# Kernel optimization log

Measured on AMD Instinct MI355X. Metric: run time of the kernel, lower is better.

Reference implementation:

```python
import jax, jax.numpy as jnp
import numpy as np

D_MODEL = 1024
NUM_HEADS = 16
D_K = D_MODEL // NUM_HEADS
THETA = 10000.0
MAX_SEQ_LEN = 2048
BATCH = 2
SEQ = 2048


def setup_inputs() -> dict:
    key = jax.random.key(0)
    ks = jax.random.split(key, 5)
    std = np.sqrt(2.0 / (D_MODEL + D_MODEL)).astype(np.float32)
    x = jax.random.normal(ks[0], (BATCH, SEQ, D_MODEL), dtype=jnp.float32)
    Wq = jax.random.normal(ks[1], (D_MODEL, D_MODEL), dtype=jnp.float32) * std
    Wk = jax.random.normal(ks[2], (D_MODEL, D_MODEL), dtype=jnp.float32) * std
    Wv = jax.random.normal(ks[3], (D_MODEL, D_MODEL), dtype=jnp.float32) * std
    Wo = jax.random.normal(ks[4], (D_MODEL, D_MODEL), dtype=jnp.float32) * std
    token_positions = jnp.arange(SEQ, dtype=jnp.int32)
    return {"x": x, "token_positions": token_positions,
            "Wq": Wq, "Wk": Wk, "Wv": Wv, "Wo": Wo}


def _rope_tables(positions):
    # freqs: [d_k/2]; angles: [seq, d_k/2]
    freqs = 1.0 / (THETA ** (jnp.arange(0, D_K, 2, dtype=jnp.float32) / D_K))
    angles = positions.astype(jnp.float32)[:, None] * freqs[None, :]
    return jnp.cos(angles), jnp.sin(angles)


def _apply_rope(t, cos, sin):
    # t: [b, h, s, d_k]; cos/sin: [s, d_k/2]; interleaved pair rotation
    x1 = t[..., 0::2]
    x2 = t[..., 1::2]
    r1 = x1 * cos - x2 * sin
    r2 = x1 * sin + x2 * cos
    return jnp.stack([r1, r2], axis=-1).reshape(t.shape)


def reference(x, token_positions, Wq, Wk, Wv, Wo):
    b, s, _ = x.shape
    # projections: y = x W^T
    q = jnp.einsum('bsi,oi->bso', x, Wq)
    k = jnp.einsum('bsi,oi->bso', x, Wk)
    v = jnp.einsum('bsi,oi->bso', x, Wv)
    # split heads: [b, h, s, d]
    q = q.reshape(b, s, NUM_HEADS, D_K).transpose(0, 2, 1, 3)
    k = k.reshape(b, s, NUM_HEADS, D_K).transpose(0, 2, 1, 3)
    v = v.reshape(b, s, NUM_HEADS, D_K).transpose(0, 2, 1, 3)
    cos, sin = _rope_tables(token_positions)
    q = _apply_rope(q, cos, sin)
    k = _apply_rope(k, cos, sin)
    scale = jnp.asarray(D_K, jnp.float32) ** 0.5
    scores = jnp.einsum('bhqd,bhkd->bhqk', q, k) / scale
    causal = jnp.tril(jnp.ones((s, s), dtype=bool))
    scores = jnp.where(causal, scores, -jnp.inf)
    attn = jax.nn.softmax(scores.astype(jnp.float32), axis=-1).astype(scores.dtype)
    out = jnp.einsum('bhqk,bhkd->bhqd', attn, v)
    out = out.transpose(0, 2, 1, 3).reshape(b, s, D_MODEL)
    return jnp.einsum('bsi,oi->bso', out, Wo)
```

## Files before the change

### kernel.cpp

```cpp
#include <hip/hip_runtime.h>
#include <stdint.h>

#define D_MODEL 1024
#define NH      16
#define DKH     64
#define SEQLEN  2048
#define BATCH   2
#define KDIM    1024

typedef __attribute__((ext_vector_type(8))) short          short8;
typedef __attribute__((ext_vector_type(4))) short          bf16x4;
typedef __attribute__((ext_vector_type(8))) unsigned short ushort8;
typedef __attribute__((ext_vector_type(4))) unsigned short usht4;
typedef __attribute__((ext_vector_type(4))) float          f32x4;

#define QSCALE 0.18033688011112042f

__device__ __forceinline__ unsigned short f2bf(float f) {
    union { float f; unsigned u; } v; v.f = f;
    unsigned u = v.u;
    unsigned r = (u + 0x7FFFu + ((u >> 16) & 1u)) >> 16;
    return (unsigned short)r;
}
__device__ __forceinline__ unsigned fbits(float f) {
    union { float f; unsigned u; } v; v.f = f; return v.u;
}

__device__ __forceinline__ void gload_lds16(const unsigned short* g, unsigned short* l) {
    __builtin_amdgcn_global_load_lds(
        (__attribute__((address_space(1))) void*)(g),
        (__attribute__((address_space(3))) void*)(l), 16, 0, 0);
}

__global__ void cvt_all(const float* __restrict__ X,  const float* __restrict__ Wq,
                        const float* __restrict__ Wk, const float* __restrict__ Wv,
                        const float* __restrict__ Wo, const int* __restrict__ pos,
                        unsigned short* __restrict__ Xb,  unsigned short* __restrict__ Wqb,
                        unsigned short* __restrict__ Wkb, unsigned short* __restrict__ Wvb,
                        unsigned short* __restrict__ Wob, float2* __restrict__ tbl) {
    const int z = blockIdx.y;
    if (z == 5) {
        int i = blockIdx.x * 256 + threadIdx.x;
        if (i < 65536) {
            int s = i >> 5, j = i & 31;
            float freq = expf(-((float)(2 * j) * (1.0f / 64.0f)) * 9.210340371976184f);
            float ang = (float)pos[s] * freq;
            float sn, cn;
            sincosf(ang, &sn, &cn);
            tbl[i] = make_float2(cn, sn);
        }
        return;
    }
    const float* src; unsigned short* dst; int n;
    if (z == 0)      { src = X;  dst = Xb;  n = 4194304; }
    else if (z == 1) { src = Wq; dst = Wqb; n = 1048576; }
    else if (z == 2) { src = Wk; dst = Wkb; n = 1048576; }
    else if (z == 3) { src = Wv; dst = Wvb; n = 1048576; }
    else             { src = Wo; dst = Wob; n = 1048576; }
    int i = (blockIdx.x * 256 + threadIdx.x) * 8;
    if (i >= n) return;
    float4 a = *(const float4*)(src + i);
    float4 b = *(const float4*)(src + i + 4);
    ushort8 o;
    o[0] = f2bf(a.x); o[1] = f2bf(a.y); o[2] = f2bf(a.z); o[3] = f2bf(a.w);
    o[4] = f2bf(b.x); o[5] = f2bf(b.y); o[6] = f2bf(b.z); o[7] = f2bf(b.w);
    *(ushort8*)(dst + i) = o;
}

__device__ __forceinline__ void gemm_core_128(
    const unsigned short* __restrict__ A, const unsigned short* __restrict__ W,
    unsigned short* a_lds, unsigned short* b_lds,
    int m0, int n0, f32x4 acc[4][4])
{
    const int tid  = threadIdx.x;
    const int lane = tid & 63;
    const int w    = tid >> 6;
    const int quad = lane >> 4;
    const int l16  = lane & 15;
    const int wm   = w & 1, wn = w >> 1;

    const int row_in = lane >> 3;
    const int cg     = ((lane & 7) ^ row_in) * 8;

    #pragma unroll
    for (int mi = 0; mi < 4; mi++)
        #pragma unroll
        for (int ni = 0; ni < 4; ni++) {
            f32x4 z = {0.f, 0.f, 0.f, 0.f};
            acc[mi][ni] = z;
        }

    const int x7 = l16 & 7;

    for (int kk = 0; kk < KDIM; kk += 64) {
        __syncthreads();
        #pragma unroll
        for (int j = 0; j < 4; ++j) {
            int c = w * 4 + j;
            gload_lds16(A + (size_t)(m0 + c * 8 + row_in) * KDIM + kk + cg, &a_lds[c * 512]);
            gload_lds16(W + (size_t)(n0 + c * 8 + row_in) * KDIM + kk + cg, &b_lds[c * 512]);
        }
        __syncthreads();

        short8 af[2][4], bf[2][4];
        #pragma unroll
        for (int kk2 = 0; kk2 < 2; kk2++)
            #pragma unroll
            for (int i = 0; i < 4; i++) {
                int g = (kk2 * 4 + quad) ^ x7;
                af[kk2][i] = *(const short8*)&a_lds[(wm * 64 + i * 16 + l16) * 64 + g * 8];
                bf[kk2][i] = *(const short8*)&b_lds[(wn * 64 + i * 16 + l16) * 64 + g * 8];
            }
        #pragma unroll
        for (int kk2 = 0; kk2 < 2; kk2++)
            #pragma unroll
            for (int mi = 0; mi < 4; mi++)
                #pragma unroll
                for (int ni = 0; ni < 4; ni++)
                    acc[mi][ni] = __builtin_amdgcn_mfma_f32_16x16x32_bf16(af[kk2][mi], bf[kk2][ni], acc[mi][ni], 0, 0, 0);
    }
}

__device__ __forceinline__ void gemm_core_128x64_db(
    const unsigned short* __restrict__ A, const unsigned short* __restrict__ W,
    unsigned short* a_lds, unsigned short* b_lds,
    int m0, int n0, f32x4 acc[4][2])
{
    const int tid  = threadIdx.x;
    const int lane = tid & 63;
    const int w    = tid >> 6;
    const int quad = lane >> 4;
    const int l16  = lane & 15;
    const int wm   = w & 1, wn = w >> 1;

    const int row_in = lane >> 3;
    const int cg     = ((lane & 7) ^ row_in) * 8;

    #pragma unroll
    for (int mi = 0; mi < 4; mi++)
        #pragma unroll
        for (int ni = 0; ni < 2; ni++) {
            f32x4 z = {0.f, 0.f, 0.f, 0.f};
            acc[mi][ni] = z;
        }

    const int x7 = l16 & 7;

    #pragma unroll
    for (int j = 0; j < 4; ++j) {
        int c = w * 4 + j;
        gload_lds16(A + (size_t)(m0 + c * 8 + row_in) * KDIM + cg, &a_lds[c * 512]);
    }
    #pragma unroll
    for (int j = 0; j < 2; ++j) {
        int c = w * 2 + j;
        gload_lds16(W + (size_t)(n0 + c * 8 + row_in) * KDIM + cg, &b_lds[c * 512]);
    }
    __syncthreads();

    int cur = 0;
    for (int kk = 0; kk < KDIM; kk += 64) {
        if (kk + 64 < KDIM) {
            const int nxt = cur ^ 1;
            #pragma unroll
            for (int j = 0; j < 4; ++j) {
                int c = w * 4 + j;
                gload_lds16(A + (size_t)(m0 + c * 8 + row_in) * KDIM + kk + 64 + cg,
                            &a_lds[nxt * 8192 + c * 512]);
            }
            #pragma unroll
            for (int j = 0; j < 2; ++j) {
                int c = w * 2 + j;
                gload_lds16(W + (size_t)(n0 + c * 8 + row_in) * KDIM + kk + 64 + cg,
                            &b_lds[nxt * 4096 + c * 512]);
            }
        }

        const unsigned short* al = &a_lds[cur * 8192];
        const unsigned short* bl = &b_lds[cur * 4096];
        short8 af[2][4], bf[2][2];
        #pragma unroll
        for (int kk2 = 0; kk2 < 2; kk2++) {
            #pragma unroll
            for (int i = 0; i < 4; i++) {
                int g = (kk2 * 4 + quad) ^ x7;
                af[kk2][i] = *(const short8*)&al[(wm * 64 + i * 16 + l16) * 64 + g * 8];
            }
            #pragma unroll
            for (int i = 0; i < 2; i++) {
                int g = (kk2 * 4 + quad) ^ x7;
                bf[kk2][i] = *(const short8*)&bl[(wn * 32 + i * 16 + l16) * 64 + g * 8];
            }
        }
        #pragma unroll
        for (int kk2 = 0; kk2 < 2; kk2++)
            #pragma unroll
            for (int mi = 0; mi < 4; mi++)
                #pragma unroll
                for (int ni = 0; ni < 2; ni++)
                    acc[mi][ni] = __builtin_amdgcn_mfma_f32_16x16x32_bf16(af[kk2][mi], bf[kk2][ni], acc[mi][ni], 0, 0, 0);

        __syncthreads();
        cur ^= 1;
    }
}

__global__ __launch_bounds__(256, 2)
void gemm_qkv(const unsigned short* __restrict__ X,
              const unsigned short* __restrict__ Wq,
              const unsigned short* __restrict__ Wk,
              const unsigned short* __restrict__ Wv,
              const float2* __restrict__ tbl,
              unsigned short* __restrict__ q_ws,
              unsigned short* __restrict__ k_ws,
              unsigned short* __restrict__ v_ws)
{
    __shared__ __align__(16) unsigned short a_lds[128 * 64];
    __shared__ __align__(16) unsigned short b_lds[128 * 64];
    __shared__ __align__(16) unsigned short t_lds[32 * 136];

    const int z = blockIdx.z;
    const unsigned short* W = (z == 0) ? Wq : ((z == 1) ? Wk : Wv);
    const int m0 = blockIdx.x * 128, n0 = blockIdx.y * 128;

    f32x4 acc[4][4];
    gemm_core_128(X, W, a_lds, b_lds, m0, n0, acc);

    const int tid  = threadIdx.x;
    const int lane = tid & 63;
    const int w    = tid >> 6;
    const int quad = lane >> 4;
    const int l16  = lane & 15;
    const int wm   = w & 1, wn = w >> 1;

    if (z == 2) {
        const int bx = m0 >> 11;
        const int c_local_w = wn * 16 + l16;
        const int rd_c = tid >> 3;
        const int rd_s = (tid & 7) * 16;
        #pragma unroll
        for (int ni = 0; ni < 4; ni++) {
            __syncthreads();
            #pragma unroll
            for (int mi = 0; mi < 4; mi++) {
                usht4 v4;
                #pragma unroll
                for (int r = 0; r < 4; r++) v4[r] = f2bf(acc[mi][ni][r]);
                *(usht4*)&t_lds[c_local_w * 136 + wm * 64 + mi * 16 + quad * 4] = v4;
            }
            __syncthreads();
            int col = n0 + (rd_c >> 4) * 64 + ni * 16 + (rd_c & 15);
            int h = col >> 6, d = col & 63;
            size_t base = (size_t)(bx * NH + h) * DKH * SEQLEN + (size_t)d * SEQLEN
                        + (m0 & 2047) + rd_s;
            ushort8 x0 = *(ushort8*)&t_lds[rd_c * 136 + rd_s];
            ushort8 x1 = *(ushort8*)&t_lds[rd_c * 136 + rd_s + 8];
            *(ushort8*)&v_ws[base]     = x0;
            *(ushort8*)&v_ws[base + 8] = x1;
        }
    } else {
        unsigned short* dst = (z == 0) ? q_ws : k_ws;
        const float sc = (z == 0) ? QSCALE : 1.0f;
        #pragma unroll
        for (int mi = 0; mi < 4; mi++)
            #pragma unroll
            for (int ni = 0; ni < 4; ni++)
                #pragma unroll
                for (int r = 0; r < 4; r++) {
                    int row = m0 + wm * 64 + mi * 16 + quad * 4 + r;
                    int col = n0 + wn * 64 + ni * 16 + l16;
                    int b = row >> 11, s = row & 2047;
                    int h = col >> 6,  d = col & 63;
                    float val = acc[mi][ni][r];
                    float other = __shfl_xor(val, 1);
                    float2 cs = tbl[s * 32 + (d >> 1)];
                    float rv = (d & 1) ? (other * cs.y + val * cs.x)
                                       : (val * cs.x - other * cs.y);
                    dst[(size_t)(b * NH + h) * SEQLEN * DKH + (size_t)s * DKH + d] =
                        f2bf(rv * sc);
                }
    }
}

__global__ __launch_bounds__(512, 2)
void attn_kernel(const unsigned short* __restrict__ q_ws,
                 const unsigned short* __restrict__ k_ws,
                 const unsigned short* __restrict__ v_ws,
                 unsigned short* __restrict__ ao)
{
    __shared__ __align__(16) unsigned short smem[17920];
    unsigned short* k_lds = smem;
    unsigned short* v_lds = smem + 128 * 72;
    float* redO = (float*)smem;
    float* redL = redO + 8192;

    const int bh  = blockIdx.x;
    const int y   = blockIdx.y;
    const int qt2 = (y < 8) ? y : (23 - y);
    const int tid = threadIdx.x, lane = tid & 63, w = tid >> 6;
    const int quad = lane >> 4, l16 = lane & 15;
    const int g   = w >> 2;
    const int w4  = w & 3;
    const int nf0 = g * 4;

    const size_t kqbase = (size_t)bh * SEQLEN * DKH;
    const size_t vbase  = (size_t)bh * DKH * SEQLEN;
    const int b = bh >> 4, h = bh & 15;

    const int krow = tid >> 3, kcol = (tid & 7) * 8;
    const int vrow = tid >> 4, vcol = (tid & 15) * 8;

    const int q0  = qt2 * 128;
    const int nt  = qt2 + 1;
    const int qwbase = q0 + w4 * 32;

    short8 aq[2][2];
    #pragma unroll
    for (int st = 0; st < 2; st++)
        #pragma unroll
        for (int kc = 0; kc < 2; kc++)
            aq[st][kc] = *(const short8*)(q_ws + kqbase +
                (size_t)(qwbase + st * 16 + l16) * DKH + kc * 32 + quad * 8);

    f32x4 o_acc[2][4];
    #pragma unroll
    for (int st = 0; st < 2; st++)
        #pragma unroll
        for (int df = 0; df < 4; df++) { f32x4 z = {0.f,0.f,0.f,0.f}; o_acc[st][df] = z; }
    float lsum[2] = {0.f, 0.f};

    ushort8 kreg[2], vreg[2];
    #pragma unroll
    for (int rr = 0; rr < 2; ++rr) {
        kreg[rr] = *(const ushort8*)(k_ws + kqbase + (size_t)(krow + rr * 64) * DKH + kcol);
        vreg[rr] = *(const ushort8*)(v_ws + vbase + (size_t)(vrow + rr * 32) * SEQLEN + vcol);
    }

    for (int t = 0; t < nt; ++t) {
        const int s0 = t * 128;
        __syncthreads();
        #pragma unroll
        for (int rr = 0; rr < 2; ++rr) {
            *(ushort8*)&k_lds[(krow + rr * 64) * 72 + kcol]  = kreg[rr];
            *(ushort8*)&v_lds[(vrow + rr * 32) * 136 + vcol] = vreg[rr];
        }
        __syncthreads();
        if (t < nt - 1) {
            int s1 = s0 + 128;
            #pragma unroll
            for (int rr = 0; rr < 2; ++rr) {
                kreg[rr] = *(const ushort8*)(k_ws + kqbase + (size_t)(s1 + krow + rr * 64) * DKH + kcol);
                vreg[rr] = *(const ushort8*)(v_ws + vbase + (size_t)(vrow + rr * 32) * SEQLEN + s1 + vcol);
            }
        }

        const bool diag = (t == nt - 1);
        #pragma unroll
        for (int nfi = 0; nfi < 4; nfi++) {
            const int nf = nf0 + nfi;
            short8 kf0 = *(const short8*)&k_lds[(nf * 16 + l16) * 72 + 0 * 32 + quad * 8];
            short8 kf1 = *(const short8*)&k_lds[(nf * 16 + l16) * 72 + 1 * 32 + quad * 8];
            bf16x4 vf[4];
            #pragma unroll
            for (int df = 0; df < 4; df++)
                vf[df] = *(const bf16x4*)&v_lds[(df * 16 + l16) * 136 + nf * 16 + quad * 4];

            #pragma unroll
            for (int st = 0; st < 2; st++) {
                f32x4 s = {0.f,0.f,0.f,0.f};
                s = __builtin_amdgcn_mfma_f32_16x16x32_bf16(kf0, aq[st][0], s, 0, 0, 0);
                s = __builtin_amdgcn_mfma_f32_16x16x32_bf16(kf1, aq[st][1], s, 0, 0, 0);

                if (diag) {
                    int qg = qwbase + st * 16 + l16;
                    int kg = s0 + nf * 16 + quad * 4;
                    #pragma unroll
                    for (int r = 0; r < 4; r++)
                        s[r] = (kg + r <= qg) ? __builtin_amdgcn_exp2f(s[r]) : 0.f;
                } else {
                    #pragma unroll
                    for (int r = 0; r < 4; r++)
                        s[r] = __builtin_amdgcn_exp2f(s[r]);
                }
                lsum[st] += s[0] + s[1] + s[2] + s[3];

                union { unsigned u[2]; bf16x4 v; } pk;
                pk.u[0] = __builtin_amdgcn_perm(fbits(s[1]), fbits(s[0]), 0x07060302u);
                pk.u[1] = __builtin_amdgcn_perm(fbits(s[3]), fbits(s[2]), 0x07060302u);

                #pragma unroll
                for (int df = 0; df < 4; df++)
                    o_acc[st][df] = __builtin_amdgcn_mfma_f32_16x16x16bf16_1k(vf[df], pk.v, o_acc[st][df], 0, 0, 0);
            }
        }
    }

    __syncthreads();
    if (g == 1) {
        #pragma unroll
        for (int st = 0; st < 2; st++) {
            #pragma unroll
            for (int df = 0; df < 4; df++)
                *(f32x4*)&redO[(((w4 * 2 + st) * 4 + df) << 8) + lane * 4] = o_acc[st][df];
            redL[(w4 * 2 + st) * 64 + lane] = lsum[st];
        }
    }
    __syncthreads();
    if (g == 0) {
        #pragma unroll
        for (int st = 0; st < 2; st++) {
            #pragma unroll
            for (int df = 0; df < 4; df++) {
                f32x4 o1 = *(const f32x4*)&redO[(((w4 * 2 + st) * 4 + df) << 8) + lane * 4];
                o_acc[st][df] += o1;
            }
            float rs = lsum[st] + redL[(w4 * 2 + st) * 64 + lane];
            rs += __shfl_xor(rs, 16);
            rs += __shfl_xor(rs, 32);
            float inv = 1.0f / rs;
            int qg = qwbase + st * 16 + l16;
            #pragma unroll
            for (int df = 0; df < 4; df++) {
                usht4 ov;
                #pragma unroll
                for (int r = 0; r < 4; r++) ov[r] = f2bf(o_acc[st][df][r] * inv);
                *(usht4*)&ao[(size_t)(b * SEQLEN + qg) * D_MODEL + h * DKH + df * 16 + quad * 4] = ov;
            }
        }
    }
}

__global__ __launch_bounds__(256, 2)
void gemm_out(const unsigned short* __restrict__ AO,
              const unsigned short* __restrict__ Wo,
              float* __restrict__ out)
{
    __shared__ __align__(16) unsigned short a_lds[2 * 128 * 64];
    __shared__ __align__(16) unsigned short b_lds[2 * 64 * 64];

    const int m0 = blockIdx.x * 128, n0 = blockIdx.y * 64;
    f32x4 acc[4][2];
    gemm_core_128x64_db(AO, Wo, a_lds, b_lds, m0, n0, acc);

    const int lane = threadIdx.x & 63;
    const int w    = threadIdx.x >> 6;
    const int quad = lane >> 4;
    const int l16  = lane & 15;
    const int wm   = w & 1, wn = w >> 1;

    #pragma unroll
    for (int mi = 0; mi < 4; mi++)
        #pragma unroll
        for (int ni = 0; ni < 2; ni++)
            #pragma unroll
            for (int r = 0; r < 4; r++) {
                int row = m0 + wm * 64 + mi * 16 + quad * 4 + r;
                int col = n0 + wn * 32 + ni * 16 + l16;
                out[(size_t)row * D_MODEL + col] = acc[mi][ni][r];
            }
}

extern "C" void kernel_launch(void* const* d_in, const int* in_sizes, int n_in,
                              void* d_out, int out_size, void* d_ws, size_t ws_size,
                              hipStream_t stream) {
    const float* X  = (const float*)d_in[0];
    const int*   pos = (const int*)d_in[1];
    const float* Wq = (const float*)d_in[2];
    const float* Wk = (const float*)d_in[3];
    const float* Wv = (const float*)d_in[4];
    const float* Wo = (const float*)d_in[5];
    float* out = (float*)d_out;

    unsigned short* Xb  = (unsigned short*)d_ws;
    unsigned short* Wqb = Xb + 4194304;
    unsigned short* Wkb = Wqb + 1048576;
    unsigned short* Wvb = Wkb + 1048576;
    unsigned short* Wob = Wvb + 1048576;
    unsigned short* q_ws = Wob + 1048576;
    unsigned short* k_ws = q_ws + 4194304;
    unsigned short* v_ws = k_ws + 4194304;
    unsigned short* ao   = v_ws + 4194304;
    float2* tbl = (float2*)(ao + 4194304);

    cvt_all<<<dim3(2048, 6), dim3(256), 0, stream>>>(X, Wq, Wk, Wv, Wo, pos,
                                                     Xb, Wqb, Wkb, Wvb, Wob, tbl);
    gemm_qkv<<<dim3(32, 8, 3), dim3(256), 0, stream>>>(Xb, Wqb, Wkb, Wvb, tbl, q_ws, k_ws, v_ws);
    attn_kernel<<<dim3(32, 16), dim3(512), 0, stream>>>(q_ws, k_ws, v_ws, ao);
    gemm_out<<<dim3(32, 16), dim3(256), 0, stream>>>(ao, Wob, out);
}
```

Baseline: 163.1 us.

## Use 512-thread QKV GEMM blocks and double-buffer K/V tiles in attention

The QKV projection kernel now launches 512 threads (8 waves) per 128x128 tile. Each wave computes a 64x32 sub-tile with fewer accumulators, which aims to raise occupancy and latency hiding; the V-transpose epilogue is reworked to match. The attention kernel double-buffers its K/V LDS tiles, so each step needs one barrier instead of two and the next tile's LDS store overlaps the current compute. The cost is doubled attention LDS use, which may cut blocks per CU, and more barrier participants in the GEMM.

```diff
diff --git a/kernel.cpp b/kernel.cpp
--- a/kernel.cpp
+++ b/kernel.cpp
@@ -67,60 +67,6 @@
     *(ushort8*)(dst + i) = o;
 }
 
-__device__ __forceinline__ void gemm_core_128(
-    const unsigned short* __restrict__ A, const unsigned short* __restrict__ W,
-    unsigned short* a_lds, unsigned short* b_lds,
-    int m0, int n0, f32x4 acc[4][4])
-{
-    const int tid  = threadIdx.x;
-    const int lane = tid & 63;
-    const int w    = tid >> 6;
-    const int quad = lane >> 4;
-    const int l16  = lane & 15;
-    const int wm   = w & 1, wn = w >> 1;
-
-    const int row_in = lane >> 3;
-    const int cg     = ((lane & 7) ^ row_in) * 8;
-
-    #pragma unroll
-    for (int mi = 0; mi < 4; mi++)
-        #pragma unroll
-        for (int ni = 0; ni < 4; ni++) {
-            f32x4 z = {0.f, 0.f, 0.f, 0.f};
-            acc[mi][ni] = z;
-        }
-
-    const int x7 = l16 & 7;
-
-    for (int kk = 0; kk < KDIM; kk += 64) {
-        __syncthreads();
-        #pragma unroll
-        for (int j = 0; j < 4; ++j) {
-            int c = w * 4 + j;
-            gload_lds16(A + (size_t)(m0 + c * 8 + row_in) * KDIM + kk + cg, &a_lds[c * 512]);
-            gload_lds16(W + (size_t)(n0 + c * 8 + row_in) * KDIM + kk + cg, &b_lds[c * 512]);
-        }
-        __syncthreads();
-
-        short8 af[2][4], bf[2][4];
-        #pragma unroll
-        for (int kk2 = 0; kk2 < 2; kk2++)
-            #pragma unroll
-            for (int i = 0; i < 4; i++) {
-                int g = (kk2 * 4 + quad) ^ x7;
-                af[kk2][i] = *(const short8*)&a_lds[(wm * 64 + i * 16 + l16) * 64 + g * 8];
-                bf[kk2][i] = *(const short8*)&b_lds[(wn * 64 + i * 16 + l16) * 64 + g * 8];
-            }
-        #pragma unroll
-        for (int kk2 = 0; kk2 < 2; kk2++)
-            #pragma unroll
-            for (int mi = 0; mi < 4; mi++)
-                #pragma unroll
-                for (int ni = 0; ni < 4; ni++)
-                    acc[mi][ni] = __builtin_amdgcn_mfma_f32_16x16x32_bf16(af[kk2][mi], bf[kk2][ni], acc[mi][ni], 0, 0, 0);
-    }
-}
-
 __device__ __forceinline__ void gemm_core_128x64_db(
     const unsigned short* __restrict__ A, const unsigned short* __restrict__ W,
     unsigned short* a_lds, unsigned short* b_lds,
@@ -205,7 +151,7 @@
     }
 }
 
-__global__ __launch_bounds__(256, 2)
+__global__ __launch_bounds__(512, 4)
 void gemm_qkv(const unsigned short* __restrict__ X,
               const unsigned short* __restrict__ Wq,
               const unsigned short* __restrict__ Wk,
@@ -223,40 +169,84 @@
     const unsigned short* W = (z == 0) ? Wq : ((z == 1) ? Wk : Wv);
     const int m0 = blockIdx.x * 128, n0 = blockIdx.y * 128;
 
-    f32x4 acc[4][4];
-    gemm_core_128(X, W, a_lds, b_lds, m0, n0, acc);
-
     const int tid  = threadIdx.x;
     const int lane = tid & 63;
     const int w    = tid >> 6;
     const int quad = lane >> 4;
     const int l16  = lane & 15;
-    const int wm   = w & 1, wn = w >> 1;
+    const int wm   = w & 1;
+    const int wn   = w >> 1;
+
+    const int row_in = lane >> 3;
+    const int cg     = ((lane & 7) ^ row_in) * 8;
+    const int x7     = l16 & 7;
+
+    f32x4 acc[4][2];
+    #pragma unroll
+    for (int mi = 0; mi < 4; mi++)
+        #pragma unroll
+        for (int ni = 0; ni < 2; ni++) {
+            f32x4 zz = {0.f, 0.f, 0.f, 0.f};
+            acc[mi][ni] = zz;
+        }
+
+    for (int kk = 0; kk < KDIM; kk += 64) {
+        __syncthreads();
+        #pragma unroll
+        for (int j = 0; j < 2; ++j) {
+            int c = w * 2 + j;
+            gload_lds16(X + (size_t)(m0 + c * 8 + row_in) * KDIM + kk + cg, &a_lds[c * 512]);
+            gload_lds16(W + (size_t)(n0 + c * 8 + row_in) * KDIM + kk + cg, &b_lds[c * 512]);
+        }
+        __syncthreads();
+
+        short8 af[2][4], bf[2][2];
+        #pragma unroll
+        for (int kk2 = 0; kk2 < 2; kk2++) {
+            #pragma unroll
+            for (int i = 0; i < 4; i++) {
+                int g = (kk2 * 4 + quad) ^ x7;
+                af[kk2][i] = *(const short8*)&a_lds[(wm * 64 + i * 16 + l16) * 64 + g * 8];
+            }
+            #pragma unroll
+            for (int i = 0; i < 2; i++) {
+                int g = (kk2 * 4 + quad) ^ x7;
+                bf[kk2][i] = *(const short8*)&b_lds[(wn * 32 + i * 16 + l16) * 64 + g * 8];
+            }
+        }
+        #pragma unroll
+        for (int kk2 = 0; kk2 < 2; kk2++)
+            #pragma unroll
+            for (int mi = 0; mi < 4; mi++)
+                #pragma unroll
+                for (int ni = 0; ni < 2; ni++)
+                    acc[mi][ni] = __builtin_amdgcn_mfma_f32_16x16x32_bf16(af[kk2][mi], bf[kk2][ni], acc[mi][ni], 0, 0, 0);
+    }
 
     if (z == 2) {
         const int bx = m0 >> 11;
-        const int c_local_w = wn * 16 + l16;
-        const int rd_c = tid >> 3;
-        const int rd_s = (tid & 7) * 16;
-        #pragma unroll
-        for (int ni = 0; ni < 4; ni++) {
+        const int rd_c = tid >> 4;
+        const int rd_s = (tid & 15) * 8;
+        #pragma unroll
+        for (int p = 0; p < 4; p++) {
             __syncthreads();
-            #pragma unroll
-            for (int mi = 0; mi < 4; mi++) {
-                usht4 v4;
-                #pragma unroll
-                for (int r = 0; r < 4; r++) v4[r] = f2bf(acc[mi][ni][r]);
-                *(usht4*)&t_lds[c_local_w * 136 + wm * 64 + mi * 16 + quad * 4] = v4;
+            if (wn == p) {
+                #pragma unroll
+                for (int mi = 0; mi < 4; mi++)
+                    #pragma unroll
+                    for (int ni = 0; ni < 2; ni++) {
+                        usht4 v4;
+                        #pragma unroll
+                        for (int r = 0; r < 4; r++) v4[r] = f2bf(acc[mi][ni][r]);
+                        *(usht4*)&t_lds[(ni * 16 + l16) * 136 + wm * 64 + mi * 16 + quad * 4] = v4;
+                    }
             }
             __syncthreads();
-            int col = n0 + (rd_c >> 4) * 64 + ni * 16 + (rd_c & 15);
+            int col = n0 + p * 32 + rd_c;
             int h = col >> 6, d = col & 63;
             size_t base = (size_t)(bx * NH + h) * DKH * SEQLEN + (size_t)d * SEQLEN
                         + (m0 & 2047) + rd_s;
-            ushort8 x0 = *(ushort8*)&t_lds[rd_c * 136 + rd_s];
-            ushort8 x1 = *(ushort8*)&t_lds[rd_c * 136 + rd_s + 8];
-            *(ushort8*)&v_ws[base]     = x0;
-            *(ushort8*)&v_ws[base + 8] = x1;
+            *(ushort8*)&v_ws[base] = *(ushort8*)&t_lds[rd_c * 136 + rd_s];
         }
     } else {
         unsigned short* dst = (z == 0) ? q_ws : k_ws;
@@ -264,11 +254,11 @@
         #pragma unroll
         for (int mi = 0; mi < 4; mi++)
             #pragma unroll
-            for (int ni = 0; ni < 4; ni++)
+            for (int ni = 0; ni < 2; ni++)
                 #pragma unroll
                 for (int r = 0; r < 4; r++) {
                     int row = m0 + wm * 64 + mi * 16 + quad * 4 + r;
-                    int col = n0 + wn * 64 + ni * 16 + l16;
+                    int col = n0 + wn * 32 + ni * 16 + l16;
                     int b = row >> 11, s = row & 2047;
                     int h = col >> 6,  d = col & 63;
                     float val = acc[mi][ni][r];
@@ -288,9 +278,7 @@
                  const unsigned short* __restrict__ v_ws,
                  unsigned short* __restrict__ ao)
 {
-    __shared__ __align__(16) unsigned short smem[17920];
-    unsigned short* k_lds = smem;
-    unsigned short* v_lds = smem + 128 * 72;
+    __shared__ __align__(16) unsigned short smem[2 * 17920];
     float* redO = (float*)smem;
     float* redL = redO + 8192;
 
@@ -318,9 +306,9 @@
     #pragma unroll
     for (int st = 0; st < 2; st++)
         #pragma unroll
-        for (int kc = 0; kc < 2; kc++)
-            aq[st][kc] = *(const short8*)(q_ws + kqbase +
-                (size_t)(qwbase + st * 16 + l16) * DKH + kc * 32 + quad * 8);
+        for (int kc2 = 0; kc2 < 2; kc2++)
+            aq[st][kc2] = *(const short8*)(q_ws + kqbase +
+                (size_t)(qwbase + st * 16 + l16) * DKH + kc2 * 32 + quad * 8);
 
     f32x4 o_acc[2][4];
     #pragma unroll
@@ -335,16 +323,22 @@
         kreg[rr] = *(const ushort8*)(k_ws + kqbase + (size_t)(krow + rr * 64) * DKH + kcol);
         vreg[rr] = *(const ushort8*)(v_ws + vbase + (size_t)(vrow + rr * 32) * SEQLEN + vcol);
     }
+    {
+        unsigned short* k0 = smem;
+        unsigned short* v0 = smem + 128 * 72;
+        #pragma unroll
+        for (int rr = 0; rr < 2; ++rr) {
+            *(ushort8*)&k0[(krow + rr * 64) * 72 + kcol]  = kreg[rr];
+            *(ushort8*)&v0[(vrow + rr * 32) * 136 + vcol] = vreg[rr];
+        }
+    }
+    __syncthreads();
 
     for (int t = 0; t < nt; ++t) {
         const int s0 = t * 128;
-        __syncthreads();
-        #pragma unroll
-        for (int rr = 0; rr < 2; ++rr) {
-            *(ushort8*)&k_lds[(krow + rr * 64) * 72 + kcol]  = kreg[rr];
-            *(ushort8*)&v_lds[(vrow + rr * 32) * 136 + vcol] = vreg[rr];
-        }
-        __syncthreads();
+        unsigned short* kc = smem + (t & 1) * 17920;
+        unsigned short* vc = kc + 128 * 72;
+
         if (t < nt - 1) {
             int s1 = s0 + 128;
             #pragma unroll
@@ -358,12 +352,12 @@
         #pragma unroll
         for (int nfi = 0; nfi < 4; nfi++) {
             const int nf = nf0 + nfi;
-            short8 kf0 = *(const short8*)&k_lds[(nf * 16 + l16) * 72 + 0 * 32 + quad * 8];
-            short8 kf1 = *(const short8*)&k_lds[(nf * 16 + l16) * 72 + 1 * 32 + quad * 8];
+            short8 kf0 = *(const short8*)&kc[(nf * 16 + l16) * 72 + 0 * 32 + quad * 8];
+            short8 kf1 = *(const short8*)&kc[(nf * 16 + l16) * 72 + 1 * 32 + quad * 8];
             bf16x4 vf[4];
             #pragma unroll
             for (int df = 0; df < 4; df++)
-                vf[df] = *(const bf16x4*)&v_lds[(df * 16 + l16) * 136 + nf * 16 + quad * 4];
+                vf[df] = *(const bf16x4*)&vc[(df * 16 + l16) * 136 + nf * 16 + quad * 4];
 
             #pragma unroll
             for (int st = 0; st < 2; st++) {
@@ -393,9 +387,19 @@
                     o_acc[st][df] = __builtin_amdgcn_mfma_f32_16x16x16bf16_1k(vf[df], pk.v, o_acc[st][df], 0, 0, 0);
             }
         }
-    }
-
-    __syncthreads();
+
+        if (t < nt - 1) {
+            unsigned short* kn = smem + ((t + 1) & 1) * 17920;
+            unsigned short* vn = kn + 128 * 72;
+            #pragma unroll
+            for (int rr = 0; rr < 2; ++rr) {
+                *(ushort8*)&kn[(krow + rr * 64) * 72 + kcol]  = kreg[rr];
+                *(ushort8*)&vn[(vrow + rr * 32) * 136 + vcol] = vreg[rr];
+            }
+        }
+        __syncthreads();
+    }
+
     if (g == 1) {
         #pragma unroll
         for (int st = 0; st < 2; st++) {
@@ -484,7 +488,7 @@
 
     cvt_all<<<dim3(2048, 6), dim3(256), 0, stream>>>(X, Wq, Wk, Wv, Wo, pos,
                                                      Xb, Wqb, Wkb, Wvb, Wob, tbl);
-    gemm_qkv<<<dim3(32, 8, 3), dim3(256), 0, stream>>>(Xb, Wqb, Wkb, Wvb, tbl, q_ws, k_ws, v_ws);
+    gemm_qkv<<<dim3(32, 8, 3), dim3(512), 0, stream>>>(Xb, Wqb, Wkb, Wvb, tbl, q_ws, k_ws, v_ws);
     attn_kernel<<<dim3(32, 16), dim3(512), 0, stream>>>(q_ws, k_ws, v_ws, ao);
     gemm_out<<<dim3(32, 16), dim3(256), 0, stream>>>(ao, Wob, out);
 }
```

Measured after the change: 171.6 us. +5.2%, slower.
